# Performance work log

Hardware: AMD Instinct MI355X
Metric: run time of the kernel (lower is better)

The kernel has to match this reference:

```python
import jax, jax.numpy as jnp
import numpy as np

B, CDD, HIS, T, L, D, K = 64, 5, 100, 30, 3, 256, 10
THRESHOLD = 0.1


def setup_inputs() -> dict:
    key = jax.random.key(0)
    k1, k2, k3, k4 = jax.random.split(key, 4)
    cdd_repr = jax.random.normal(k1, (B, CDD, D), dtype=jnp.float32)
    his_repr = jax.random.normal(k2, (B, HIS, D), dtype=jnp.float32)
    his_embedding = jax.random.normal(k3, (B, HIS, T, L, D), dtype=jnp.float32)
    # xavier_normal init for Linear(D, D)
    W_sel = jax.random.normal(k4, (D, D), dtype=jnp.float32) * np.sqrt(2.0 / (D + D))
    b_sel = jnp.zeros((D,), dtype=jnp.float32)
    return {"cdd_repr": cdd_repr, "his_repr": his_repr,
            "his_embedding": his_embedding, "W_sel": W_sel, "b_sel": b_sel}


def _l2_normalize(x, eps=1e-12):
    # matches torch F.normalize(dim=-1)
    n = jnp.linalg.norm(x, axis=-1, keepdims=True)
    return x / jnp.maximum(n, eps)


def reference(cdd_repr, his_repr, his_embedding, W_sel, b_sel):
    # selectionProject (Linear) + L2 normalize
    cdd_p = _l2_normalize(cdd_repr @ W_sel.T + b_sel)   # [B, CDD, D]
    his_p = _l2_normalize(his_repr @ W_sel.T + b_sel)   # [B, HIS, D]

    # news-level attention scores [B, CDD, HIS]
    attn = jnp.einsum('bcd,bhd->bch', cdd_p, his_p)

    # top-k over history
    attn_topk, idx = jax.lax.top_k(attn, K)             # [B, CDD, K]

    # multi-dim gather of history embeddings -> [B, CDD, K, T, L, D]
    his_activated = his_embedding[jnp.arange(B)[:, None, None], idx]

    # threshold masking: zero out weights below threshold, scale embeddings
    w = jnp.where(attn_topk < THRESHOLD, 0.0, attn_topk)
    his_activated = his_activated * w[:, :, :, None, None, None]

    return his_activated, idx
```

## Files before the change

kernel.cpp:

```cpp
#include <hip/hip_runtime.h>
#include <hip/hip_bf16.h>

#define NB   64
#define NCDD 5
#define NHIS 100
#define ND   256
#define NK   10
#define TLD  23040
#define THRESH 0.1f
#define NEG_INF (-3.402823466e38f)
#define NROWS_HIS 6400
#define NROWS_CDD 320

typedef float f32x4 __attribute__((ext_vector_type(4)));

__global__ __launch_bounds__(256) void proj_norm_all(
    const float* __restrict__ his_repr,
    const float* __restrict__ cdd_repr,
    const float* __restrict__ W,
    const float* __restrict__ bvec,
    float* __restrict__ Yall)
{
    __shared__ float red[4][16];
    const int r0  = blockIdx.x * 16;
    const int tid = threadIdx.x;

    const float* __restrict__ X = (r0 < NROWS_HIS)
        ? (his_repr + (size_t)r0 * ND)
        : (cdd_repr + (size_t)(r0 - NROWS_HIS) * ND);

    const float bias = bvec[tid];
    float acc[16];
#pragma unroll
    for (int r = 0; r < 16; ++r) acc[r] = bias;

    const float* wrow = W + (size_t)tid * ND;
    for (int k = 0; k < ND; k += 4) {
        const float4 w4 = *(const float4*)(wrow + k);
#pragma unroll
        for (int r = 0; r < 16; ++r) {
            const float4 x4 = *(const float4*)(X + (size_t)r * ND + k);
            acc[r] += w4.x * x4.x + w4.y * x4.y + w4.z * x4.z + w4.w * x4.w;
        }
    }

    const int wave = tid >> 6, lane = tid & 63;
#pragma unroll
    for (int r = 0; r < 16; ++r) {
        float v = acc[r] * acc[r];
        for (int off = 32; off; off >>= 1) v += __shfl_xor(v, off);
        if (lane == 0) red[wave][r] = v;
    }
    __syncthreads();

#pragma unroll
    for (int r = 0; r < 16; ++r) {
        const float s = red[0][r] + red[1][r] + red[2][r] + red[3][r];
        const float scale = 1.0f / fmaxf(sqrtf(s), 1e-12f);
        Yall[(size_t)(r0 + r) * ND + tid] = acc[r] * scale;
    }
}

__global__ __launch_bounds__(256) void attn_topk_kernel(
    const float* __restrict__ cdd_p,
    const float* __restrict__ his_p,
    float* __restrict__ out_idx_f,
    int* __restrict__ ws_idx,
    float* __restrict__ ws_w)
{
    __shared__ float cvec[ND];
    __shared__ float attn_s[NHIS];
    const int bc  = blockIdx.x;
    const int b   = bc / NCDD;
    const int tid = threadIdx.x;
    const int wave = tid >> 6, lane = tid & 63;

    cvec[tid] = cdd_p[(size_t)bc * ND + tid];
    __syncthreads();

    const float4 c4 = ((const float4*)cvec)[lane];
    for (int h = wave; h < NHIS; h += 4) {
        const float4 h4 =
            ((const float4*)(his_p + ((size_t)b * NHIS + h) * ND))[lane];
        float v = c4.x * h4.x + c4.y * h4.y + c4.z * h4.z + c4.w * h4.w;
        for (int off = 32; off; off >>= 1) v += __shfl_xor(v, off);
        if (lane == 0) attn_s[h] = v;
    }
    __syncthreads();

    if (wave == 0) {
        float v0 = attn_s[lane];
        float v1 = (lane + 64 < NHIS) ? attn_s[lane + 64] : NEG_INF;
#pragma unroll
        for (int k = 0; k < NK; ++k) {
            float lv; int li;
            if (v1 > v0) { lv = v1; li = lane + 64; }
            else         { lv = v0; li = lane; }
            for (int off = 1; off < 64; off <<= 1) {
                const float ov = __shfl_xor(lv, off);
                const int   oi = __shfl_xor(li, off);
                if (ov > lv || (ov == lv && oi < li)) { lv = ov; li = oi; }
            }
            if (lane == 0) {
                const float w = (lv < THRESH) ? 0.0f : lv;
                const int g = bc * NK + k;
                ws_idx[g] = li;
                ws_w[g]   = w;
                out_idx_f[g] = (float)li;
            }
            if (li == lane)            v0 = NEG_INF;
            else if (li == lane + 64)  v1 = NEG_INF;
        }
    }
}

__global__ __launch_bounds__(256) void gather_kernel(
    const float* __restrict__ his_emb,
    const int* __restrict__ ws_idx,
    const float* __restrict__ ws_w,
    float* __restrict__ out)
{
    const int orig = blockIdx.x;
    const int g = (orig & 7) * 400 + (orig >> 3);
    const int b = g / (NCDD * NK);
    const int tid = threadIdx.x;
    const float w = ws_w[g];

    f32x4* __restrict__ dst = (f32x4*)(out + (size_t)g * TLD);

    if (w == 0.0f) {
        const f32x4 z = {0.f, 0.f, 0.f, 0.f};
#pragma unroll
        for (int it = 0; it < 22; ++it) dst[tid + it * 256] = z;
        if (tid < 128) dst[22 * 256 + tid] = z;
        return;
    }

    const int idx = ws_idx[g];
    const f32x4* __restrict__ src =
        (const f32x4*)(his_emb + ((size_t)b * NHIS + idx) * TLD);

    f32x4 v[8];
#pragma unroll
    for (int j = 0; j < 8; ++j) v[j] = src[tid + j * 256];
#pragma unroll
    for (int j = 0; j < 8; ++j) dst[tid + j * 256] = v[j] * w;
#pragma unroll
    for (int j = 0; j < 8; ++j) v[j] = src[tid + (8 + j) * 256];
#pragma unroll
    for (int j = 0; j < 8; ++j) dst[tid + (8 + j) * 256] = v[j] * w;
#pragma unroll
    for (int j = 0; j < 6; ++j) v[j] = src[tid + (16 + j) * 256];
#pragma unroll
    for (int j = 0; j < 6; ++j) dst[tid + (16 + j) * 256] = v[j] * w;
    if (tid < 128) {
        const int i = 22 * 256 + tid;
        f32x4 t = src[i];
        dst[i] = t * w;
    }
}

extern "C" void kernel_launch(void* const* d_in, const int* in_sizes, int n_in,
                              void* d_out, int out_size, void* d_ws, size_t ws_size,
                              hipStream_t stream)
{
    const float* cdd_repr = (const float*)d_in[0];
    const float* his_repr = (const float*)d_in[1];
    const float* his_emb  = (const float*)d_in[2];
    const float* W_sel    = (const float*)d_in[3];
    const float* b_sel    = (const float*)d_in[4];
    float* out = (float*)d_out;

    char* ws = (char*)d_ws;
    float* Yall  = (float*)ws;
    float* his_p = Yall;
    float* cdd_p = Yall + (size_t)NROWS_HIS * ND;
    int*   idx_i = (int*)  (ws + 6881280);
    float* w_w   = (float*)(ws + 6894080);

    float* out_idx_f = out + (size_t)NB * NCDD * NK * TLD;

    proj_norm_all<<<(NROWS_HIS + NROWS_CDD) / 16, 256, 0, stream>>>(
        his_repr, cdd_repr, W_sel, b_sel, Yall);
    attn_topk_kernel<<<NB * NCDD, 256, 0, stream>>>(cdd_p, his_p,
                                                    out_idx_f, idx_i, w_w);
    gather_kernel<<<NB * NCDD * NK, 256, 0, stream>>>(his_emb, idx_i, w_w, out);
}
```

Measured before the change: 176.6 us.

## Halve projection rows per block and restructure attention to one block per batch

The projection kernel now handles 8 rows per block instead of 16, doubling the grid to 840 blocks for better CU occupancy. The attention/top-k kernel is reorganized so each 512-thread block processes all 5 candidates of one batch. Each thread computes one full candidate-history dot product serially from shared memory, replacing per-wave shuffle reductions, and five waves then run top-k in parallel. This trades 320 small blocks for 64 larger ones, which may underuse the GPU, and the long per-thread serial dot products reading uncoalesced history rows could cost latency.

Measured after the change: 173.3 us. About the same (-1.9%).

```diff
diff --git a/kernel.cpp b/kernel.cpp
--- a/kernel.cpp
+++ b/kernel.cpp
@@ -21,8 +21,8 @@
     const float* __restrict__ bvec,
     float* __restrict__ Yall)
 {
-    __shared__ float red[4][16];
-    const int r0  = blockIdx.x * 16;
+    __shared__ float red[4][8];
+    const int r0  = blockIdx.x * 8;
     const int tid = threadIdx.x;
 
     const float* __restrict__ X = (r0 < NROWS_HIS)
@@ -30,15 +30,15 @@
         : (cdd_repr + (size_t)(r0 - NROWS_HIS) * ND);
 
     const float bias = bvec[tid];
-    float acc[16];
+    float acc[8];
 #pragma unroll
-    for (int r = 0; r < 16; ++r) acc[r] = bias;
+    for (int r = 0; r < 8; ++r) acc[r] = bias;
 
     const float* wrow = W + (size_t)tid * ND;
     for (int k = 0; k < ND; k += 4) {
         const float4 w4 = *(const float4*)(wrow + k);
 #pragma unroll
-        for (int r = 0; r < 16; ++r) {
+        for (int r = 0; r < 8; ++r) {
             const float4 x4 = *(const float4*)(X + (size_t)r * ND + k);
             acc[r] += w4.x * x4.x + w4.y * x4.y + w4.z * x4.z + w4.w * x4.w;
         }
@@ -46,7 +46,7 @@
 
     const int wave = tid >> 6, lane = tid & 63;
 #pragma unroll
-    for (int r = 0; r < 16; ++r) {
+    for (int r = 0; r < 8; ++r) {
         float v = acc[r] * acc[r];
         for (int off = 32; off; off >>= 1) v += __shfl_xor(v, off);
         if (lane == 0) red[wave][r] = v;
@@ -54,43 +54,54 @@
     __syncthreads();
 
 #pragma unroll
-    for (int r = 0; r < 16; ++r) {
+    for (int r = 0; r < 8; ++r) {
         const float s = red[0][r] + red[1][r] + red[2][r] + red[3][r];
         const float scale = 1.0f / fmaxf(sqrtf(s), 1e-12f);
         Yall[(size_t)(r0 + r) * ND + tid] = acc[r] * scale;
     }
 }
 
-__global__ __launch_bounds__(256) void attn_topk_kernel(
+__global__ __launch_bounds__(512) void attn_topk_kernel(
     const float* __restrict__ cdd_p,
     const float* __restrict__ his_p,
     float* __restrict__ out_idx_f,
     int* __restrict__ ws_idx,
     float* __restrict__ ws_w)
 {
-    __shared__ float cvec[ND];
-    __shared__ float attn_s[NHIS];
-    const int bc  = blockIdx.x;
-    const int b   = bc / NCDD;
+    __shared__ f32x4 cdds[NCDD * 64];
+    __shared__ float attn_s[NCDD][128];
+    const int b   = blockIdx.x;
     const int tid = threadIdx.x;
-    const int wave = tid >> 6, lane = tid & 63;
 
-    cvec[tid] = cdd_p[(size_t)bc * ND + tid];
+    for (int i = tid; i < NCDD * 64; i += 512)
+        cdds[i] = ((const f32x4*)(cdd_p + (size_t)b * NCDD * ND))[i];
     __syncthreads();
 
-    const float4 c4 = ((const float4*)cvec)[lane];
-    for (int h = wave; h < NHIS; h += 4) {
-        const float4 h4 =
-            ((const float4*)(his_p + ((size_t)b * NHIS + h) * ND))[lane];
-        float v = c4.x * h4.x + c4.y * h4.y + c4.z * h4.z + c4.w * h4.w;
-        for (int off = 32; off; off >>= 1) v += __shfl_xor(v, off);
-        if (lane == 0) attn_s[h] = v;
+    if (tid < NCDD * NHIS) {
+        const int c = tid / NHIS, h = tid % NHIS;
+        const f32x4* __restrict__ hrow =
+            (const f32x4*)(his_p + ((size_t)b * NHIS + h) * ND);
+        float a0 = 0.f, a1 = 0.f, a2 = 0.f, a3 = 0.f;
+#pragma unroll 8
+        for (int k = 0; k < 64; k += 4) {
+            const f32x4 c0 = cdds[c * 64 + k],     h0 = hrow[k];
+            const f32x4 c1 = cdds[c * 64 + k + 1], h1 = hrow[k + 1];
+            const f32x4 c2 = cdds[c * 64 + k + 2], h2 = hrow[k + 2];
+            const f32x4 c3 = cdds[c * 64 + k + 3], h3 = hrow[k + 3];
+            a0 += c0[0]*h0[0] + c0[1]*h0[1] + c0[2]*h0[2] + c0[3]*h0[3];
+            a1 += c1[0]*h1[0] + c1[1]*h1[1] + c1[2]*h1[2] + c1[3]*h1[3];
+            a2 += c2[0]*h2[0] + c2[1]*h2[1] + c2[2]*h2[2] + c2[3]*h2[3];
+            a3 += c3[0]*h3[0] + c3[1]*h3[1] + c3[2]*h3[2] + c3[3]*h3[3];
+        }
+        attn_s[c][h] = (a0 + a1) + (a2 + a3);
     }
     __syncthreads();
 
-    if (wave == 0) {
-        float v0 = attn_s[lane];
-        float v1 = (lane + 64 < NHIS) ? attn_s[lane + 64] : NEG_INF;
+    const int wave = tid >> 6, lane = tid & 63;
+    if (wave < NCDD) {
+        const int c = wave;
+        float v0 = attn_s[c][lane];
+        float v1 = (lane + 64 < NHIS) ? attn_s[c][lane + 64] : NEG_INF;
 #pragma unroll
         for (int k = 0; k < NK; ++k) {
             float lv; int li;
@@ -103,7 +114,7 @@
             }
             if (lane == 0) {
                 const float w = (lv < THRESH) ? 0.0f : lv;
-                const int g = bc * NK + k;
+                const int g = (b * NCDD + c) * NK + k;
                 ws_idx[g] = li;
                 ws_w[g]   = w;
                 out_idx_f[g] = (float)li;
@@ -180,9 +191,9 @@
 
     float* out_idx_f = out + (size_t)NB * NCDD * NK * TLD;
 
-    proj_norm_all<<<(NROWS_HIS + NROWS_CDD) / 16, 256, 0, stream>>>(
+    proj_norm_all<<<(NROWS_HIS + NROWS_CDD) / 8, 256, 0, stream>>>(
         his_repr, cdd_repr, W_sel, b_sel, Yall);
-    attn_topk_kernel<<<NB * NCDD, 256, 0, stream>>>(cdd_p, his_p,
-                                                    out_idx_f, idx_i, w_w);
+    attn_topk_kernel<<<NB, 512, 0, stream>>>(cdd_p, his_p,
+                                             out_idx_f, idx_i, w_w);
     gather_kernel<<<NB * NCDD * NK, 256, 0, stream>>>(his_emb, idx_i, w_w, out);
 }
```

## Stage transposed W tiles in LDS for projection; one attention block per batch

Applied to the files above, without the earlier changes.

The projection kernel now loads W in 32-column tiles into a transposed, padded shared-memory buffer, so each thread reads its weights from LDS with a conflict-free stride instead of doing strided per-thread row loads from global memory. The attention/top-k kernel is regrouped so each 512-thread block handles all 5 candidates of one batch, sharing the history rows across candidates and running five top-k waves in parallel. This adds two barriers per K tile and cuts the attention grid to 64 blocks, which may underuse the GPU. The gather kernel, which likely dominates time, is unchanged.

Measured after the change: 298.1 us. 68.8% more time.

```diff
diff --git a/kernel.cpp b/kernel.cpp
--- a/kernel.cpp
+++ b/kernel.cpp
@@ -21,6 +21,7 @@
     const float* __restrict__ bvec,
     float* __restrict__ Yall)
 {
+    __shared__ float wt[32][257];
     __shared__ float red[4][16];
     const int r0  = blockIdx.x * 16;
     const int tid = threadIdx.x;
@@ -34,14 +35,34 @@
 #pragma unroll
     for (int r = 0; r < 16; ++r) acc[r] = bias;
 
-    const float* wrow = W + (size_t)tid * ND;
-    for (int k = 0; k < ND; k += 4) {
-        const float4 w4 = *(const float4*)(wrow + k);
-#pragma unroll
-        for (int r = 0; r < 16; ++r) {
-            const float4 x4 = *(const float4*)(X + (size_t)r * ND + k);
-            acc[r] += w4.x * x4.x + w4.y * x4.y + w4.z * x4.z + w4.w * x4.w;
+    for (int kt = 0; kt < 8; ++kt) {
+        const int k0 = kt * 32;
+#pragma unroll
+        for (int j = 0; j < 8; ++j) {
+            const int f   = tid + j * 256;
+            const int d   = f >> 3;
+            const int kk4 = (f & 7) << 2;
+            const float4 w4 = *(const float4*)(W + (size_t)d * ND + k0 + kk4);
+            wt[kk4 + 0][d] = w4.x;
+            wt[kk4 + 1][d] = w4.y;
+            wt[kk4 + 2][d] = w4.z;
+            wt[kk4 + 3][d] = w4.w;
         }
+        __syncthreads();
+
+#pragma unroll
+        for (int j = 0; j < 8; ++j) {
+            const float w0 = wt[4 * j + 0][tid];
+            const float w1 = wt[4 * j + 1][tid];
+            const float w2 = wt[4 * j + 2][tid];
+            const float w3 = wt[4 * j + 3][tid];
+#pragma unroll
+            for (int r = 0; r < 16; ++r) {
+                const float4 x4 = *(const float4*)(X + (size_t)r * ND + k0 + 4 * j);
+                acc[r] += x4.x * w0 + x4.y * w1 + x4.z * w2 + x4.w * w3;
+            }
+        }
+        __syncthreads();
     }
 
     const int wave = tid >> 6, lane = tid & 63;
@@ -61,36 +82,39 @@
     }
 }
 
-__global__ __launch_bounds__(256) void attn_topk_kernel(
+__global__ __launch_bounds__(512) void attn_topk_kernel(
     const float* __restrict__ cdd_p,
     const float* __restrict__ his_p,
     float* __restrict__ out_idx_f,
     int* __restrict__ ws_idx,
     float* __restrict__ ws_w)
 {
-    __shared__ float cvec[ND];
-    __shared__ float attn_s[NHIS];
-    const int bc  = blockIdx.x;
-    const int b   = bc / NCDD;
+    __shared__ f32x4 cdds[NCDD * 64];
+    __shared__ float attn_s[NCDD][128];
+    const int b   = blockIdx.x;
     const int tid = threadIdx.x;
     const int wave = tid >> 6, lane = tid & 63;
 
-    cvec[tid] = cdd_p[(size_t)bc * ND + tid];
+    for (int i = tid; i < NCDD * 64; i += 512)
+        cdds[i] = ((const f32x4*)(cdd_p + (size_t)b * NCDD * ND))[i];
     __syncthreads();
 
-    const float4 c4 = ((const float4*)cvec)[lane];
-    for (int h = wave; h < NHIS; h += 4) {
-        const float4 h4 =
-            ((const float4*)(his_p + ((size_t)b * NHIS + h) * ND))[lane];
-        float v = c4.x * h4.x + c4.y * h4.y + c4.z * h4.z + c4.w * h4.w;
+    for (int idx = wave; idx < NCDD * NHIS; idx += 8) {
+        const int c = idx / NHIS, h = idx - c * NHIS;
+        const f32x4 cv = cdds[c * 64 + lane];
+        const f32x4 hv =
+            ((const f32x4*)(his_p + ((size_t)b * NHIS + h) * ND))[lane];
+        float v = cv[0] * hv[0] + cv[1] * hv[1] + cv[2] * hv[2] + cv[3] * hv[3];
+#pragma unroll
         for (int off = 32; off; off >>= 1) v += __shfl_xor(v, off);
-        if (lane == 0) attn_s[h] = v;
+        if (lane == 0) attn_s[c][h] = v;
     }
     __syncthreads();
 
-    if (wave == 0) {
-        float v0 = attn_s[lane];
-        float v1 = (lane + 64 < NHIS) ? attn_s[lane + 64] : NEG_INF;
+    if (wave < NCDD) {
+        const int c = wave;
+        float v0 = attn_s[c][lane];
+        float v1 = (lane + 64 < NHIS) ? attn_s[c][lane + 64] : NEG_INF;
 #pragma unroll
         for (int k = 0; k < NK; ++k) {
             float lv; int li;
@@ -103,7 +127,7 @@
             }
             if (lane == 0) {
                 const float w = (lv < THRESH) ? 0.0f : lv;
-                const int g = bc * NK + k;
+                const int g = (b * NCDD + c) * NK + k;
                 ws_idx[g] = li;
                 ws_w[g]   = w;
                 out_idx_f[g] = (float)li;
@@ -182,7 +206,7 @@
 
     proj_norm_all<<<(NROWS_HIS + NROWS_CDD) / 16, 256, 0, stream>>>(
         his_repr, cdd_repr, W_sel, b_sel, Yall);
-    attn_topk_kernel<<<NB * NCDD, 256, 0, stream>>>(cdd_p, his_p,
-                                                    out_idx_f, idx_i, w_w);
+    attn_topk_kernel<<<NB, 512, 0, stream>>>(cdd_p, his_p,
+                                             out_idx_f, idx_i, w_w);
     gather_kernel<<<NB * NCDD * NK, 256, 0, stream>>>(his_emb, idx_i, w_w, out);
 }
```
